# Kernel tuning notes

Hardware: AMD Instinct MI355X
Metric: run time of the kernel (lower is better)

The kernel has to match this reference:

```python
import math
import jax, jax.numpy as jnp
import numpy as np

B, S, HID = 2, 2048, 1024
H, D = 16, 64
LOG2E = 1.442695041


def setup_inputs() -> dict:
    key = jax.random.key(0)
    ks = jax.random.split(key, 10)
    init = lambda k, shape, fan_in: jax.random.uniform(k, shape, jnp.float32, -1.0, 1.0) / math.sqrt(fan_in)
    hidden_states = jax.random.normal(ks[0], (B, S, HID), jnp.float32)
    # additive causal mask [B, 1, S, S]: 0 on/below diagonal, large negative above
    neg = jnp.finfo(jnp.float32).min
    causal = jnp.where(jnp.tril(jnp.ones((S, S), bool)), 0.0, neg).astype(jnp.float32)
    attention_mask = jnp.broadcast_to(causal[None, None], (B, 1, S, S))
    return {
        "hidden_states": hidden_states,
        "attention_mask": attention_mask,
        "scaling": jax.random.normal(ks[1], (D,), jnp.float32) * 0.1,
        "q_w": init(ks[2], (H * D, HID), HID),
        "q_b": jnp.zeros((H * D,), jnp.float32),
        "k_w": init(ks[3], (H * D, HID), HID),
        "k_b": jnp.zeros((H * D,), jnp.float32),
        "v_w": init(ks[4], (H * D, HID), HID),
        "v_b": jnp.zeros((H * D,), jnp.float32),
        "o_w": init(ks[5], (HID, H * D), H * D),
        "o_b": jnp.zeros((HID,), jnp.float32),
    }


def reference(hidden_states, attention_mask, scaling, q_w, q_b, k_w, k_b, v_w, v_b, o_w, o_b):
    x = hidden_states  # [B, S, HID]
    def proj(w, b):
        y = jnp.einsum('bsh,oh->bso', x, w) + b          # [B, S, H*D]
        return y.reshape(B, S, H, D).transpose(0, 2, 1, 3)  # [B, H, S, D]
    q = proj(q_w, q_b)
    k = proj(k_w, k_b)
    v = proj(v_w, v_b)
    # learned per-head-dim softplus scale on queries
    scale = jax.nn.softplus(scaling) * (LOG2E / math.sqrt(D))  # [D]
    q = q * scale[None, None, None, :]
    attn = jnp.einsum('bhsd,bhtd->bhst', q, k)  # [B, H, S, S]
    attn = attn + attention_mask
    attn = jax.nn.softmax(attn.astype(jnp.float32), axis=-1).astype(q.dtype)
    # dropout p=0.0 / eval mode: no-op
    out = jnp.einsum('bhst,bhtd->bhsd', attn, v)           # [B, H, S, D]
    out = out.transpose(0, 2, 1, 3).reshape(B, S, H * D)   # [B, S, H*D]
    out = jnp.einsum('bsf,of->bso', out, o_w) + o_b        # [B, S, HID]
    return out, attn
```

## Files before the change

### kernel.cpp

```cpp
#include <hip/hip_runtime.h>
#include <hip/hip_bf16.h>

#define BATCH 2
#define SEQ   2048
#define HIDN  1024
#define NH    16
#define HD    64

typedef __attribute__((ext_vector_type(8))) short short8;
typedef __attribute__((ext_vector_type(4))) float floatx4;
typedef __attribute__((ext_vector_type(8))) unsigned short ushort8;

__device__ __forceinline__ unsigned short f2bf(float f) {
    union { float f; unsigned int u; } v; v.f = f;
    unsigned int u = v.u;
    u += 0x7fffu + ((u >> 16) & 1u);
    return (unsigned short)(u >> 16);
}

__device__ __forceinline__ ushort8 pack16(float4 f0, float4 f1) {
    ushort8 r;
    r[0] = f2bf(f0.x); r[1] = f2bf(f0.y); r[2] = f2bf(f0.z); r[3] = f2bf(f0.w);
    r[4] = f2bf(f1.x); r[5] = f2bf(f1.y); r[6] = f2bf(f1.z); r[7] = f2bf(f1.w);
    return r;
}

__global__ __launch_bounds__(256) void qkv_kernel(
    const float* __restrict__ x,
    const float* __restrict__ qw, const float* __restrict__ qbias,
    const float* __restrict__ kw, const float* __restrict__ kbias,
    const float* __restrict__ vw, const float* __restrict__ vbias,
    const float* __restrict__ scaling,
    unsigned short* __restrict__ qo,
    unsigned short* __restrict__ ko,
    unsigned short* __restrict__ vo)
{
    const int z = blockIdx.z;
    const float* w    = (z == 0) ? qw : (z == 1) ? kw : vw;
    const float* bias = (z == 0) ? qbias : (z == 1) ? kbias : vbias;
    unsigned short* dst = (z == 0) ? qo : (z == 1) ? ko : vo;

    const int n0 = blockIdx.x * 128;
    const int m0 = blockIdx.y * 128;
    const int tid  = threadIdx.x;
    const int lane = tid & 63;
    const int wv   = tid >> 6;
    const int nidx = lane & 15;
    const int quad = lane >> 4;

    __shared__ unsigned short As[128][40];
    __shared__ unsigned short Bs[128][40];

    floatx4 acc[2][8];
#pragma unroll
    for (int rt = 0; rt < 2; rt++)
#pragma unroll
        for (int ct = 0; ct < 8; ct++) acc[rt][ct] = (floatx4)0.0f;

    const int srow = tid >> 1;
    const int scol = (tid & 1) * 16;

    for (int k0 = 0; k0 < HIDN; k0 += 32) {
        __syncthreads();
        {
            const float4* g = (const float4*)(x + (size_t)(m0 + srow) * HIDN + k0 + scol);
            float4 f0 = g[0], f1 = g[1], f2 = g[2], f3 = g[3];
            *(ushort8*)&As[srow][scol]     = pack16(f0, f1);
            *(ushort8*)&As[srow][scol + 8] = pack16(f2, f3);
        }
        {
            const float4* g = (const float4*)(w + (size_t)(n0 + srow) * HIDN + k0 + scol);
            float4 f0 = g[0], f1 = g[1], f2 = g[2], f3 = g[3];
            *(ushort8*)&Bs[srow][scol]     = pack16(f0, f1);
            *(ushort8*)&Bs[srow][scol + 8] = pack16(f2, f3);
        }
        __syncthreads();

        short8 a[2], bb[8];
#pragma unroll
        for (int rt = 0; rt < 2; rt++)
            a[rt] = *(const short8*)&As[wv * 32 + rt * 16 + nidx][quad * 8];
#pragma unroll
        for (int ct = 0; ct < 8; ct++)
            bb[ct] = *(const short8*)&Bs[ct * 16 + nidx][quad * 8];
#pragma unroll
        for (int rt = 0; rt < 2; rt++)
#pragma unroll
            for (int ct = 0; ct < 8; ct++)
                acc[rt][ct] = __builtin_amdgcn_mfma_f32_16x16x32_bf16(a[rt], bb[ct], acc[rt][ct], 0, 0, 0);
    }

    const float sconst = 1.442695041f / 8.0f;
#pragma unroll
    for (int ct = 0; ct < 8; ct++) {
        int col = n0 + ct * 16 + nidx;
        float bcol = bias[col];
        float mult = 1.0f;
        if (z == 0) {
            float sc = scaling[col & (HD - 1)];
            mult = __logf(1.0f + __expf(sc)) * sconst;
        }
#pragma unroll
        for (int rt = 0; rt < 2; rt++) {
#pragma unroll
            for (int rg = 0; rg < 4; rg++) {
                int row = m0 + wv * 32 + rt * 16 + quad * 4 + rg;
                float val = (acc[rt][ct][rg] + bcol) * mult;
                int b_ = row >> 11, s_ = row & (SEQ - 1);
                int h_ = col >> 6,  d_ = col & (HD - 1);
                dst[((size_t)(b_ * NH + h_) * SEQ + s_) * HD + d_] = f2bf(val);
            }
        }
    }
}

__global__ __launch_bounds__(256) void attn_kernel(
    const unsigned short* __restrict__ q,
    const unsigned short* __restrict__ k,
    const unsigned short* __restrict__ v,
    float* __restrict__ attn,
    unsigned short* __restrict__ ctx)
{
    const int qt = blockIdx.x;
    const int h  = blockIdx.y;
    const int b  = blockIdx.z;
    const int tid  = threadIdx.x;
    const int lane = tid & 63;
    const int wv   = tid >> 6;
    const int nidx = lane & 15;
    const int quad = lane >> 4;

    const unsigned short* qg = q + (size_t)((b * NH + h) * SEQ) * HD;
    const unsigned short* kg = k + (size_t)((b * NH + h) * SEQ) * HD;
    const unsigned short* vg = v + (size_t)((b * NH + h) * SEQ) * HD;
    float* ag = attn + (size_t)(b * NH + h) * SEQ * SEQ;

    __shared__ unsigned short Qs[64][72];
    __shared__ unsigned short Ks[64][72];
    __shared__ unsigned short Vs[64][72];
    __shared__ unsigned short Ps[64][72];

    const int srow = tid >> 2;
    const int sseg = tid & 3;

    {
        const uint4* g = (const uint4*)(qg + (size_t)(qt * 64 + srow) * HD);
        uint4 u0 = g[sseg], u1 = g[sseg + 4];
        *(uint4*)&Qs[srow][sseg * 8]      = u0;
        *(uint4*)&Qs[srow][sseg * 8 + 32] = u1;
    }

    const int arow  = wv * 16 + nidx;
    const int crow0 = wv * 16 + quad * 4;
    const int rowg0 = qt * 64 + crow0;

    float psum[4] = {0.f, 0.f, 0.f, 0.f};
    for (int kt = 0; kt <= qt; kt++) {
        __syncthreads();
        {
            const uint4* g = (const uint4*)(kg + (size_t)(kt * 64 + srow) * HD);
            uint4 u0 = g[sseg], u1 = g[sseg + 4];
            *(uint4*)&Ks[srow][sseg * 8]      = u0;
            *(uint4*)&Ks[srow][sseg * 8 + 32] = u1;
        }
        __syncthreads();

        short8 a0 = *(const short8*)&Qs[arow][quad * 8];
        short8 a1 = *(const short8*)&Qs[arow][32 + quad * 8];
        const bool diag = (kt == qt);
#pragma unroll
        for (int ct = 0; ct < 4; ct++) {
            floatx4 sacc = (floatx4)0.0f;
            short8 b0 = *(const short8*)&Ks[ct * 16 + nidx][quad * 8];
            short8 b1 = *(const short8*)&Ks[ct * 16 + nidx][32 + quad * 8];
            sacc = __builtin_amdgcn_mfma_f32_16x16x32_bf16(a0, b0, sacc, 0, 0, 0);
            sacc = __builtin_amdgcn_mfma_f32_16x16x32_bf16(a1, b1, sacc, 0, 0, 0);
            int colg = kt * 64 + ct * 16 + nidx;
#pragma unroll
            for (int rg = 0; rg < 4; rg++) {
                float e = __expf(sacc[rg]);
                if (diag && colg > rowg0 + rg) e = 0.0f;
                psum[rg] += e;
            }
        }
    }

    float invl[4];
#pragma unroll
    for (int rg = 0; rg < 4; rg++) {
        float s = psum[rg];
        s += __shfl_xor(s, 1);
        s += __shfl_xor(s, 2);
        s += __shfl_xor(s, 4);
        s += __shfl_xor(s, 8);
        invl[rg] = 1.0f / s;
    }

    floatx4 oacc[4];
#pragma unroll
    for (int ct = 0; ct < 4; ct++) oacc[ct] = (floatx4)0.0f;

    for (int kt = 0; kt <= qt; kt++) {
        __syncthreads();
        {
            const uint4* g = (const uint4*)(kg + (size_t)(kt * 64 + srow) * HD);
            uint4 u0 = g[sseg], u1 = g[sseg + 4];
            *(uint4*)&Ks[srow][sseg * 8]      = u0;
            *(uint4*)&Ks[srow][sseg * 8 + 32] = u1;
        }
        {
            const uint4* g = (const uint4*)(vg + (size_t)(kt * 64 + srow) * HD);
            uint4 u0 = g[sseg], u1 = g[sseg + 4];
            union { uint4 u; unsigned short s[8]; } w0, w1;
            w0.u = u0; w1.u = u1;
#pragma unroll
            for (int j = 0; j < 8; j++) Vs[sseg * 8 + j][srow]      = w0.s[j];
#pragma unroll
            for (int j = 0; j < 8; j++) Vs[sseg * 8 + 32 + j][srow] = w1.s[j];
        }
        __syncthreads();

        short8 a0 = *(const short8*)&Qs[arow][quad * 8];
        short8 a1 = *(const short8*)&Qs[arow][32 + quad * 8];
        const bool diag = (kt == qt);
#pragma unroll
        for (int ct = 0; ct < 4; ct++) {
            floatx4 sacc = (floatx4)0.0f;
            short8 b0 = *(const short8*)&Ks[ct * 16 + nidx][quad * 8];
            short8 b1 = *(const short8*)&Ks[ct * 16 + nidx][32 + quad * 8];
            sacc = __builtin_amdgcn_mfma_f32_16x16x32_bf16(a0, b0, sacc, 0, 0, 0);
            sacc = __builtin_amdgcn_mfma_f32_16x16x32_bf16(a1, b1, sacc, 0, 0, 0);
            int colg = kt * 64 + ct * 16 + nidx;
#pragma unroll
            for (int rg = 0; rg < 4; rg++) {
                float e = __expf(sacc[rg]);
                if (diag && colg > rowg0 + rg) e = 0.0f;
                ag[(size_t)(rowg0 + rg) * SEQ + colg] = e * invl[rg];
                Ps[crow0 + rg][ct * 16 + nidx] = f2bf(e);
            }
        }
        __syncthreads();

#pragma unroll
        for (int ki = 0; ki < 2; ki++) {
            short8 pa = *(const short8*)&Ps[arow][ki * 32 + quad * 8];
#pragma unroll
            for (int ct = 0; ct < 4; ct++) {
                short8 vb = *(const short8*)&Vs[ct * 16 + nidx][ki * 32 + quad * 8];
                oacc[ct] = __builtin_amdgcn_mfma_f32_16x16x32_bf16(pa, vb, oacc[ct], 0, 0, 0);
            }
        }
    }

    const int zc0 = (qt + 1) * 64;
    if (zc0 < SEQ) {
        const int zw4 = (SEQ - zc0) >> 2;
        const int total = 64 * zw4;
        for (int i = tid; i < total; i += 256) {
            int r = i / zw4;
            int c = zc0 + (i - r * zw4) * 4;
            *(float4*)&ag[(size_t)(qt * 64 + r) * SEQ + c] = make_float4(0.f, 0.f, 0.f, 0.f);
        }
    }

#pragma unroll
    for (int ct = 0; ct < 4; ct++) {
#pragma unroll
        for (int rg = 0; rg < 4; rg++) {
            int rowg = rowg0 + rg;
            int d = ct * 16 + nidx;
            float val = oacc[ct][rg] * invl[rg];
            ctx[((size_t)(b * SEQ + rowg) * NH + h) * HD + d] = f2bf(val);
        }
    }
}

__global__ __launch_bounds__(256) void oproj_kernel(
    const unsigned short* __restrict__ ctx,
    const float* __restrict__ ow, const float* __restrict__ ob,
    float* __restrict__ out)
{
    const int n0 = blockIdx.x * 128;
    const int m0 = blockIdx.y * 128;
    const int tid  = threadIdx.x;
    const int lane = tid & 63;
    const int wv   = tid >> 6;
    const int nidx = lane & 15;
    const int quad = lane >> 4;

    __shared__ unsigned short As[128][40];
    __shared__ unsigned short Bs[128][40];

    floatx4 acc[2][8];
#pragma unroll
    for (int rt = 0; rt < 2; rt++)
#pragma unroll
        for (int ct = 0; ct < 8; ct++) acc[rt][ct] = (floatx4)0.0f;

    const int srow = tid >> 1;
    const int scol = (tid & 1) * 16;

    for (int k0 = 0; k0 < HIDN; k0 += 32) {
        __syncthreads();
        {
            const uint4* g = (const uint4*)(ctx + (size_t)(m0 + srow) * HIDN + k0 + scol);
            uint4 u0 = g[0], u1 = g[1];
            *(uint4*)&As[srow][scol]     = u0;
            *(uint4*)&As[srow][scol + 8] = u1;
        }
        {
            const float4* g = (const float4*)(ow + (size_t)(n0 + srow) * HIDN + k0 + scol);
            float4 f0 = g[0], f1 = g[1], f2 = g[2], f3 = g[3];
            *(ushort8*)&Bs[srow][scol]     = pack16(f0, f1);
            *(ushort8*)&Bs[srow][scol + 8] = pack16(f2, f3);
        }
        __syncthreads();

        short8 a[2], bb[8];
#pragma unroll
        for (int rt = 0; rt < 2; rt++)
            a[rt] = *(const short8*)&As[wv * 32 + rt * 16 + nidx][quad * 8];
#pragma unroll
        for (int ct = 0; ct < 8; ct++)
            bb[ct] = *(const short8*)&Bs[ct * 16 + nidx][quad * 8];
#pragma unroll
        for (int rt = 0; rt < 2; rt++)
#pragma unroll
            for (int ct = 0; ct < 8; ct++)
                acc[rt][ct] = __builtin_amdgcn_mfma_f32_16x16x32_bf16(a[rt], bb[ct], acc[rt][ct], 0, 0, 0);
    }

#pragma unroll
    for (int ct = 0; ct < 8; ct++) {
        int col = n0 + ct * 16 + nidx;
        float bcol = ob[col];
#pragma unroll
        for (int rt = 0; rt < 2; rt++) {
#pragma unroll
            for (int rg = 0; rg < 4; rg++) {
                int row = m0 + wv * 32 + rt * 16 + quad * 4 + rg;
                out[(size_t)row * HIDN + col] = acc[rt][ct][rg] + bcol;
            }
        }
    }
}

extern "C" void kernel_launch(void* const* d_in, const int* in_sizes, int n_in,
                              void* d_out, int out_size, void* d_ws, size_t ws_size,
                              hipStream_t stream) {
    const float* x       = (const float*)d_in[0];
    const float* scaling = (const float*)d_in[2];
    const float* qw = (const float*)d_in[3];
    const float* qb = (const float*)d_in[4];
    const float* kw = (const float*)d_in[5];
    const float* kb = (const float*)d_in[6];
    const float* vw = (const float*)d_in[7];
    const float* vb = (const float*)d_in[8];
    const float* ow = (const float*)d_in[9];
    const float* ob = (const float*)d_in[10];

    float* out  = (float*)d_out;
    float* attn = out + (size_t)BATCH * SEQ * HIDN;

    const size_t per = (size_t)BATCH * NH * SEQ * HD;
    unsigned short* qbuf = (unsigned short*)d_ws;
    unsigned short* kbuf = qbuf + per;
    unsigned short* vbuf = kbuf + per;
    unsigned short* ctxb = vbuf + per;

    qkv_kernel<<<dim3(8, 32, 3), 256, 0, stream>>>(
        x, qw, qb, kw, kb, vw, vb, scaling, qbuf, kbuf, vbuf);
    attn_kernel<<<dim3(32, NH, BATCH), 256, 0, stream>>>(
        qbuf, kbuf, vbuf, attn, ctxb);
    oproj_kernel<<<dim3(8, 32), 256, 0, stream>>>(
        ctxb, ow, ob, out);
}
```

Measured before the change: 799.5 us.

## Pre-convert to bf16, unify GEMMs with direct-to-LDS swizzled loads, transpose V

Adds a conversion kernel that casts the input and all weights to bf16 once. A templated GEMM replaces both projection kernels; it stages tiles with global_load_lds into an XOR-swizzled LDS layout using K-steps of 64, and writes V transposed. The attention kernel drops LDS staging of Q/K/V and reads fragments straight from global memory, replacing barriers with compiler fences, and zero-fills the masked region row-wise per wave. This aims to cut conversion work, LDS traffic and synchronisation, at the cost of an extra kernel pass and uncoalesced global fragment reads. Removing the barriers around the shared Ps buffer is safe only because each wave writes and reads its own rows.

```diff
diff --git a/kernel.cpp b/kernel.cpp
--- a/kernel.cpp
+++ b/kernel.cpp
@@ -9,7 +9,6 @@
 
 typedef __attribute__((ext_vector_type(8))) short short8;
 typedef __attribute__((ext_vector_type(4))) float floatx4;
-typedef __attribute__((ext_vector_type(8))) unsigned short ushort8;
 
 __device__ __forceinline__ unsigned short f2bf(float f) {
     union { float f; unsigned int u; } v; v.f = f;
@@ -18,97 +17,173 @@
     return (unsigned short)(u >> 16);
 }
 
-__device__ __forceinline__ ushort8 pack16(float4 f0, float4 f1) {
-    ushort8 r;
-    r[0] = f2bf(f0.x); r[1] = f2bf(f0.y); r[2] = f2bf(f0.z); r[3] = f2bf(f0.w);
-    r[4] = f2bf(f1.x); r[5] = f2bf(f1.y); r[6] = f2bf(f1.z); r[7] = f2bf(f1.w);
-    return r;
-}
-
-__global__ __launch_bounds__(256) void qkv_kernel(
-    const float* __restrict__ x,
-    const float* __restrict__ qw, const float* __restrict__ qbias,
-    const float* __restrict__ kw, const float* __restrict__ kbias,
-    const float* __restrict__ vw, const float* __restrict__ vbias,
+__device__ __forceinline__ void glds16(const unsigned short* g, unsigned short* l) {
+    typedef const unsigned int __attribute__((address_space(1)))* gp_t;
+    typedef unsigned int __attribute__((address_space(3)))* lp_t;
+    __builtin_amdgcn_global_load_lds((gp_t)(const void*)g, (lp_t)(void*)l, 16, 0, 0);
+}
+
+__global__ __launch_bounds__(256) void convert_kernel(
+    const float* __restrict__ x,  const float* __restrict__ qw,
+    const float* __restrict__ kw, const float* __restrict__ vw,
+    const float* __restrict__ ow, unsigned short* __restrict__ dst)
+{
+    size_t i = ((size_t)blockIdx.x * 256 + threadIdx.x) * 4;
+    const float* src;
+    if (i < 4194304) {
+        src = x + i;
+    } else {
+        size_t w = i - 4194304;
+        int seg = (int)(w >> 20);
+        size_t o = w & 1048575;
+        src = (seg == 0 ? qw : seg == 1 ? kw : seg == 2 ? vw : ow) + o;
+    }
+    float4 f = *(const float4*)src;
+    ushort4 u;
+    u.x = f2bf(f.x); u.y = f2bf(f.y); u.z = f2bf(f.z); u.w = f2bf(f.w);
+    *(ushort4*)(dst + i) = u;
+}
+
+template<int MT>
+__global__ __launch_bounds__(256) void gemm_kernel(
+    const unsigned short* __restrict__ A,
+    const unsigned short* __restrict__ w0, const unsigned short* __restrict__ w1,
+    const unsigned short* __restrict__ w2,
+    const float* __restrict__ bias0, const float* __restrict__ bias1,
+    const float* __restrict__ bias2,
     const float* __restrict__ scaling,
-    unsigned short* __restrict__ qo,
-    unsigned short* __restrict__ ko,
-    unsigned short* __restrict__ vo)
+    unsigned short* __restrict__ o0, unsigned short* __restrict__ o1,
+    unsigned short* __restrict__ o2,
+    float* __restrict__ ofp,
+    int modebase)
 {
-    const int z = blockIdx.z;
-    const float* w    = (z == 0) ? qw : (z == 1) ? kw : vw;
-    const float* bias = (z == 0) ? qbias : (z == 1) ? kbias : vbias;
-    unsigned short* dst = (z == 0) ? qo : (z == 1) ? ko : vo;
+    constexpr int RT = MT / 64;
+    constexpr int IA = MT / 32;
+    const int mode = modebase + blockIdx.z;
+    const unsigned short* W = (mode == 1) ? w1 : (mode == 2) ? w2 : w0;
+    const float* bias = (mode == 1) ? bias1 : (mode == 2) ? bias2 : bias0;
 
     const int n0 = blockIdx.x * 128;
-    const int m0 = blockIdx.y * 128;
-    const int tid  = threadIdx.x;
+    const int m0 = blockIdx.y * MT;
+    const int tid = threadIdx.x;
     const int lane = tid & 63;
-    const int wv   = tid >> 6;
+    const int wv = tid >> 6;
     const int nidx = lane & 15;
     const int quad = lane >> 4;
 
-    __shared__ unsigned short As[128][40];
-    __shared__ unsigned short Bs[128][40];
-
-    floatx4 acc[2][8];
-#pragma unroll
-    for (int rt = 0; rt < 2; rt++)
+    __shared__ unsigned short As[MT * 64];
+    __shared__ unsigned short Bs[128 * 64];
+
+    floatx4 acc[RT][8];
+#pragma unroll
+    for (int rt = 0; rt < RT; rt++)
 #pragma unroll
         for (int ct = 0; ct < 8; ct++) acc[rt][ct] = (floatx4)0.0f;
 
-    const int srow = tid >> 1;
-    const int scol = (tid & 1) * 16;
-
-    for (int k0 = 0; k0 < HIDN; k0 += 32) {
+    const bool vswap = (mode == 2);
+
+    for (int k0 = 0; k0 < HIDN; k0 += 64) {
         __syncthreads();
-        {
-            const float4* g = (const float4*)(x + (size_t)(m0 + srow) * HIDN + k0 + scol);
-            float4 f0 = g[0], f1 = g[1], f2 = g[2], f3 = g[3];
-            *(ushort8*)&As[srow][scol]     = pack16(f0, f1);
-            *(ushort8*)&As[srow][scol + 8] = pack16(f2, f3);
-        }
-        {
-            const float4* g = (const float4*)(w + (size_t)(n0 + srow) * HIDN + k0 + scol);
-            float4 f0 = g[0], f1 = g[1], f2 = g[2], f3 = g[3];
-            *(ushort8*)&Bs[srow][scol]     = pack16(f0, f1);
-            *(ushort8*)&Bs[srow][scol + 8] = pack16(f2, f3);
+#pragma unroll
+        for (int i = 0; i < IA; i++) {
+            int c = (wv * IA + i) * 64 + lane;
+            int r = c >> 3;
+            int qq = (c & 7) ^ (r & 7);
+            glds16(A + (size_t)(m0 + r) * HIDN + k0 + qq * 8,
+                   As + (size_t)(wv * IA + i) * 512);
+        }
+#pragma unroll
+        for (int i = 0; i < 4; i++) {
+            int c = (wv * 4 + i) * 64 + lane;
+            int r = c >> 3;
+            int qq = (c & 7) ^ (r & 7);
+            glds16(W + (size_t)(n0 + r) * HIDN + k0 + qq * 8,
+                   Bs + (size_t)(wv * 4 + i) * 512);
         }
         __syncthreads();
 
-        short8 a[2], bb[8];
-#pragma unroll
-        for (int rt = 0; rt < 2; rt++)
-            a[rt] = *(const short8*)&As[wv * 32 + rt * 16 + nidx][quad * 8];
-#pragma unroll
-        for (int ct = 0; ct < 8; ct++)
-            bb[ct] = *(const short8*)&Bs[ct * 16 + nidx][quad * 8];
-#pragma unroll
-        for (int rt = 0; rt < 2; rt++)
-#pragma unroll
-            for (int ct = 0; ct < 8; ct++)
-                acc[rt][ct] = __builtin_amdgcn_mfma_f32_16x16x32_bf16(a[rt], bb[ct], acc[rt][ct], 0, 0, 0);
+#pragma unroll
+        for (int kc = 0; kc < 2; kc++) {
+            short8 a[RT];
+#pragma unroll
+            for (int rt = 0; rt < RT; rt++) {
+                int r = wv * (MT / 4) + rt * 16 + nidx;
+                int qq = kc * 4 + quad;
+                int chunk = r * 8 + (qq ^ (r & 7));
+                a[rt] = *(const short8*)(As + chunk * 8);
+            }
+            if (vswap) {
+#pragma unroll
+                for (int ct = 0; ct < 8; ct++) {
+                    int r = ct * 16 + nidx;
+                    int qq = kc * 4 + quad;
+                    int chunk = r * 8 + (qq ^ (r & 7));
+                    short8 bf = *(const short8*)(Bs + chunk * 8);
+#pragma unroll
+                    for (int rt = 0; rt < RT; rt++)
+                        acc[rt][ct] = __builtin_amdgcn_mfma_f32_16x16x32_bf16(bf, a[rt], acc[rt][ct], 0, 0, 0);
+                }
+            } else {
+#pragma unroll
+                for (int ct = 0; ct < 8; ct++) {
+                    int r = ct * 16 + nidx;
+                    int qq = kc * 4 + quad;
+                    int chunk = r * 8 + (qq ^ (r & 7));
+                    short8 bf = *(const short8*)(Bs + chunk * 8);
+#pragma unroll
+                    for (int rt = 0; rt < RT; rt++)
+                        acc[rt][ct] = __builtin_amdgcn_mfma_f32_16x16x32_bf16(a[rt], bf, acc[rt][ct], 0, 0, 0);
+                }
+            }
+        }
     }
 
     const float sconst = 1.442695041f / 8.0f;
 #pragma unroll
     for (int ct = 0; ct < 8; ct++) {
-        int col = n0 + ct * 16 + nidx;
-        float bcol = bias[col];
-        float mult = 1.0f;
-        if (z == 0) {
-            float sc = scaling[col & (HD - 1)];
-            mult = __logf(1.0f + __expf(sc)) * sconst;
-        }
-#pragma unroll
-        for (int rt = 0; rt < 2; rt++) {
-#pragma unroll
-            for (int rg = 0; rg < 4; rg++) {
-                int row = m0 + wv * 32 + rt * 16 + quad * 4 + rg;
-                float val = (acc[rt][ct][rg] + bcol) * mult;
-                int b_ = row >> 11, s_ = row & (SEQ - 1);
-                int h_ = col >> 6,  d_ = col & (HD - 1);
-                dst[((size_t)(b_ * NH + h_) * SEQ + s_) * HD + d_] = f2bf(val);
+        if (mode == 2) {
+#pragma unroll
+            for (int rt = 0; rt < RT; rt++) {
+#pragma unroll
+                for (int rg = 0; rg < 4; rg++) {
+                    int wrow = n0 + ct * 16 + quad * 4 + rg;
+                    int xrow = m0 + wv * (MT / 4) + rt * 16 + nidx;
+                    float val = acc[rt][ct][rg] + bias[wrow];
+                    int h_ = wrow >> 6, d_ = wrow & (HD - 1);
+                    int b_ = xrow >> 11, s_ = xrow & (SEQ - 1);
+                    o2[((size_t)(b_ * NH + h_) * HD + d_) * SEQ + s_] = f2bf(val);
+                }
+            }
+        } else if (mode == 3) {
+            int col = n0 + ct * 16 + nidx;
+            float bc = bias[col];
+#pragma unroll
+            for (int rt = 0; rt < RT; rt++) {
+#pragma unroll
+                for (int rg = 0; rg < 4; rg++) {
+                    int row = m0 + wv * (MT / 4) + rt * 16 + quad * 4 + rg;
+                    ofp[(size_t)row * HIDN + col] = acc[rt][ct][rg] + bc;
+                }
+            }
+        } else {
+            int col = n0 + ct * 16 + nidx;
+            float bc = bias[col];
+            float mult = 1.0f;
+            if (mode == 0) {
+                float sc = scaling[col & (HD - 1)];
+                mult = __logf(1.0f + __expf(sc)) * sconst;
+            }
+            unsigned short* dst = (mode == 0) ? o0 : o1;
+#pragma unroll
+            for (int rt = 0; rt < RT; rt++) {
+#pragma unroll
+                for (int rg = 0; rg < 4; rg++) {
+                    int row = m0 + wv * (MT / 4) + rt * 16 + quad * 4 + rg;
+                    float val = (acc[rt][ct][rg] + bc) * mult;
+                    int b_ = row >> 11, s_ = row & (SEQ - 1);
+                    int h_ = col >> 6,  d_ = col & (HD - 1);
+                    dst[((size_t)(b_ * NH + h_) * SEQ + s_) * HD + d_] = f2bf(val);
+                }
             }
         }
     }
@@ -117,7 +192,7 @@
 __global__ __launch_bounds__(256) void attn_kernel(
     const unsigned short* __restrict__ q,
     const unsigned short* __restrict__ k,
-    const unsigned short* __restrict__ v,
+    const unsigned short* __restrict__ vT,
     float* __restrict__ attn,
     unsigned short* __restrict__ ctx)
 {
@@ -125,54 +200,35 @@
     const int h  = blockIdx.y;
     const int b  = blockIdx.z;
     const int tid  = threadIdx.x;
+    const int wv   = (tid >> 6);
     const int lane = tid & 63;
-    const int wv   = tid >> 6;
     const int nidx = lane & 15;
     const int quad = lane >> 4;
 
-    const unsigned short* qg = q + (size_t)((b * NH + h) * SEQ) * HD;
-    const unsigned short* kg = k + (size_t)((b * NH + h) * SEQ) * HD;
-    const unsigned short* vg = v + (size_t)((b * NH + h) * SEQ) * HD;
+    const unsigned short* qg = q  + (size_t)((b * NH + h) * SEQ) * HD;
+    const unsigned short* kg = k  + (size_t)((b * NH + h) * SEQ) * HD;
+    const unsigned short* vg = vT + (size_t)((b * NH + h) * HD) * SEQ;
     float* ag = attn + (size_t)(b * NH + h) * SEQ * SEQ;
 
-    __shared__ unsigned short Qs[64][72];
-    __shared__ unsigned short Ks[64][72];
-    __shared__ unsigned short Vs[64][72];
     __shared__ unsigned short Ps[64][72];
-
-    const int srow = tid >> 2;
-    const int sseg = tid & 3;
-
-    {
-        const uint4* g = (const uint4*)(qg + (size_t)(qt * 64 + srow) * HD);
-        uint4 u0 = g[sseg], u1 = g[sseg + 4];
-        *(uint4*)&Qs[srow][sseg * 8]      = u0;
-        *(uint4*)&Qs[srow][sseg * 8 + 32] = u1;
-    }
 
     const int arow  = wv * 16 + nidx;
     const int crow0 = wv * 16 + quad * 4;
     const int rowg0 = qt * 64 + crow0;
 
+    const unsigned short* qrow = qg + (size_t)(qt * 64 + arow) * HD + quad * 8;
+    short8 a0 = *(const short8*)qrow;
+    short8 a1 = *(const short8*)(qrow + 32);
+
     float psum[4] = {0.f, 0.f, 0.f, 0.f};
     for (int kt = 0; kt <= qt; kt++) {
-        __syncthreads();
-        {
-            const uint4* g = (const uint4*)(kg + (size_t)(kt * 64 + srow) * HD);
-            uint4 u0 = g[sseg], u1 = g[sseg + 4];
-            *(uint4*)&Ks[srow][sseg * 8]      = u0;
-            *(uint4*)&Ks[srow][sseg * 8 + 32] = u1;
-        }
-        __syncthreads();
-
-        short8 a0 = *(const short8*)&Qs[arow][quad * 8];
-        short8 a1 = *(const short8*)&Qs[arow][32 + quad * 8];
         const bool diag = (kt == qt);
 #pragma unroll
         for (int ct = 0; ct < 4; ct++) {
+            const unsigned short* kr = kg + (size_t)(kt * 64 + ct * 16 + nidx) * HD + quad * 8;
+            short8 b0 = *(const short8*)kr;
+            short8 b1 = *(const short8*)(kr + 32);
             floatx4 sacc = (floatx4)0.0f;
-            short8 b0 = *(const short8*)&Ks[ct * 16 + nidx][quad * 8];
-            short8 b1 = *(const short8*)&Ks[ct * 16 + nidx][32 + quad * 8];
             sacc = __builtin_amdgcn_mfma_f32_16x16x32_bf16(a0, b0, sacc, 0, 0, 0);
             sacc = __builtin_amdgcn_mfma_f32_16x16x32_bf16(a1, b1, sacc, 0, 0, 0);
             int colg = kt * 64 + ct * 16 + nidx;
@@ -201,33 +257,13 @@
     for (int ct = 0; ct < 4; ct++) oacc[ct] = (floatx4)0.0f;
 
     for (int kt = 0; kt <= qt; kt++) {
-        __syncthreads();
-        {
-            const uint4* g = (const uint4*)(kg + (size_t)(kt * 64 + srow) * HD);
-            uint4 u0 = g[sseg], u1 = g[sseg + 4];
-            *(uint4*)&Ks[srow][sseg * 8]      = u0;
-            *(uint4*)&Ks[srow][sseg * 8 + 32] = u1;
-        }
-        {
-            const uint4* g = (const uint4*)(vg + (size_t)(kt * 64 + srow) * HD);
-            uint4 u0 = g[sseg], u1 = g[sseg + 4];
-            union { uint4 u; unsigned short s[8]; } w0, w1;
-            w0.u = u0; w1.u = u1;
-#pragma unroll
-            for (int j = 0; j < 8; j++) Vs[sseg * 8 + j][srow]      = w0.s[j];
-#pragma unroll
-            for (int j = 0; j < 8; j++) Vs[sseg * 8 + 32 + j][srow] = w1.s[j];
-        }
-        __syncthreads();
-
-        short8 a0 = *(const short8*)&Qs[arow][quad * 8];
-        short8 a1 = *(const short8*)&Qs[arow][32 + quad * 8];
         const bool diag = (kt == qt);
 #pragma unroll
         for (int ct = 0; ct < 4; ct++) {
+            const unsigned short* kr = kg + (size_t)(kt * 64 + ct * 16 + nidx) * HD + quad * 8;
+            short8 b0 = *(const short8*)kr;
+            short8 b1 = *(const short8*)(kr + 32);
             floatx4 sacc = (floatx4)0.0f;
-            short8 b0 = *(const short8*)&Ks[ct * 16 + nidx][quad * 8];
-            short8 b1 = *(const short8*)&Ks[ct * 16 + nidx][32 + quad * 8];
             sacc = __builtin_amdgcn_mfma_f32_16x16x32_bf16(a0, b0, sacc, 0, 0, 0);
             sacc = __builtin_amdgcn_mfma_f32_16x16x32_bf16(a1, b1, sacc, 0, 0, 0);
             int colg = kt * 64 + ct * 16 + nidx;
@@ -239,27 +275,28 @@
                 Ps[crow0 + rg][ct * 16 + nidx] = f2bf(e);
             }
         }
-        __syncthreads();
+        asm volatile("" ::: "memory");
 
 #pragma unroll
         for (int ki = 0; ki < 2; ki++) {
             short8 pa = *(const short8*)&Ps[arow][ki * 32 + quad * 8];
 #pragma unroll
             for (int ct = 0; ct < 4; ct++) {
-                short8 vb = *(const short8*)&Vs[ct * 16 + nidx][ki * 32 + quad * 8];
+                const unsigned short* vr = vg + (size_t)(ct * 16 + nidx) * SEQ + kt * 64 + ki * 32 + quad * 8;
+                short8 vb = *(const short8*)vr;
                 oacc[ct] = __builtin_amdgcn_mfma_f32_16x16x32_bf16(pa, vb, oacc[ct], 0, 0, 0);
             }
         }
-    }
-
-    const int zc0 = (qt + 1) * 64;
-    if (zc0 < SEQ) {
-        const int zw4 = (SEQ - zc0) >> 2;
-        const int total = 64 * zw4;
-        for (int i = tid; i < total; i += 256) {
-            int r = i / zw4;
-            int c = zc0 + (i - r * zw4) * 4;
-            *(float4*)&ag[(size_t)(qt * 64 + r) * SEQ + c] = make_float4(0.f, 0.f, 0.f, 0.f);
+        asm volatile("" ::: "memory");
+    }
+
+    {
+        const int c4start = (qt + 1) * 16;
+        const float4 z4 = make_float4(0.f, 0.f, 0.f, 0.f);
+        for (int r = wv; r < 64; r += 4) {
+            float4* rowp = (float4*)(ag + (size_t)(qt * 64 + r) * SEQ);
+            for (int c4 = c4start + lane; c4 < 512; c4 += 64)
+                rowp[c4] = z4;
         }
     }
 
@@ -271,76 +308,6 @@
             int d = ct * 16 + nidx;
             float val = oacc[ct][rg] * invl[rg];
             ctx[((size_t)(b * SEQ + rowg) * NH + h) * HD + d] = f2bf(val);
-        }
-    }
-}
-
-__global__ __launch_bounds__(256) void oproj_kernel(
-    const unsigned short* __restrict__ ctx,
-    const float* __restrict__ ow, const float* __restrict__ ob,
-    float* __restrict__ out)
-{
-    const int n0 = blockIdx.x * 128;
-    const int m0 = blockIdx.y * 128;
-    const int tid  = threadIdx.x;
-    const int lane = tid & 63;
-    const int wv   = tid >> 6;
-    const int nidx = lane & 15;
-    const int quad = lane >> 4;
-
-    __shared__ unsigned short As[128][40];
-    __shared__ unsigned short Bs[128][40];
-
-    floatx4 acc[2][8];
-#pragma unroll
-    for (int rt = 0; rt < 2; rt++)
-#pragma unroll
-        for (int ct = 0; ct < 8; ct++) acc[rt][ct] = (floatx4)0.0f;
-
-    const int srow = tid >> 1;
-    const int scol = (tid & 1) * 16;
-
-    for (int k0 = 0; k0 < HIDN; k0 += 32) {
-        __syncthreads();
-        {
-            const uint4* g = (const uint4*)(ctx + (size_t)(m0 + srow) * HIDN + k0 + scol);
-            uint4 u0 = g[0], u1 = g[1];
-            *(uint4*)&As[srow][scol]     = u0;
-            *(uint4*)&As[srow][scol + 8] = u1;
-        }
-        {
-            const float4* g = (const float4*)(ow + (size_t)(n0 + srow) * HIDN + k0 + scol);
-            float4 f0 = g[0], f1 = g[1], f2 = g[2], f3 = g[3];
-            *(ushort8*)&Bs[srow][scol]     = pack16(f0, f1);
-            *(ushort8*)&Bs[srow][scol + 8] = pack16(f2, f3);
-        }
-        __syncthreads();
-
-        short8 a[2], bb[8];
-#pragma unroll
-        for (int rt = 0; rt < 2; rt++)
-            a[rt] = *(const short8*)&As[wv * 32 + rt * 16 + nidx][quad * 8];
-#pragma unroll
-        for (int ct = 0; ct < 8; ct++)
-            bb[ct] = *(const short8*)&Bs[ct * 16 + nidx][quad * 8];
-#pragma unroll
-        for (int rt = 0; rt < 2; rt++)
-#pragma unroll
-            for (int ct = 0; ct < 8; ct++)
-                acc[rt][ct] = __builtin_amdgcn_mfma_f32_16x16x32_bf16(a[rt], bb[ct], acc[rt][ct], 0, 0, 0);
-    }
-
-#pragma unroll
-    for (int ct = 0; ct < 8; ct++) {
-        int col = n0 + ct * 16 + nidx;
-        float bcol = ob[col];
-#pragma unroll
-        for (int rt = 0; rt < 2; rt++) {
-#pragma unroll
-            for (int rg = 0; rg < 4; rg++) {
-                int row = m0 + wv * 32 + rt * 16 + quad * 4 + rg;
-                out[(size_t)row * HIDN + col] = acc[rt][ct][rg] + bcol;
-            }
         }
     }
 }
@@ -362,16 +329,26 @@
     float* out  = (float*)d_out;
     float* attn = out + (size_t)BATCH * SEQ * HIDN;
 
-    const size_t per = (size_t)BATCH * NH * SEQ * HD;
-    unsigned short* qbuf = (unsigned short*)d_ws;
-    unsigned short* kbuf = qbuf + per;
-    unsigned short* vbuf = kbuf + per;
-    unsigned short* ctxb = vbuf + per;
-
-    qkv_kernel<<<dim3(8, 32, 3), 256, 0, stream>>>(
-        x, qw, qb, kw, kb, vw, vb, scaling, qbuf, kbuf, vbuf);
+    unsigned short* xbf  = (unsigned short*)d_ws;
+    unsigned short* qwb  = xbf + 4194304;
+    unsigned short* kwb  = qwb + 1048576;
+    unsigned short* vwb  = kwb + 1048576;
+    unsigned short* owb  = vwb + 1048576;
+    unsigned short* qbuf = owb + 1048576;
+    unsigned short* kbuf = qbuf + 4194304;
+    unsigned short* vTb  = kbuf + 4194304;
+    unsigned short* ctxb = vTb + 4194304;
+
+    convert_kernel<<<8192, 256, 0, stream>>>(x, qw, kw, vw, ow, xbf);
+
+    gemm_kernel<128><<<dim3(8, 32, 3), 256, 0, stream>>>(
+        xbf, qwb, kwb, vwb, qb, kb, vb, scaling,
+        qbuf, kbuf, vTb, nullptr, 0);
+
     attn_kernel<<<dim3(32, NH, BATCH), 256, 0, stream>>>(
-        qbuf, kbuf, vbuf, attn, ctxb);
-    oproj_kernel<<<dim3(8, 32), 256, 0, stream>>>(
-        ctxb, ow, ob, out);
-}
+        qbuf, kbuf, vTb, attn, ctxb);
+
+    gemm_kernel<64><<<dim3(8, 64, 1), 256, 0, stream>>>(
+        ctxb, owb, owb, owb, ob, ob, ob, scaling,
+        nullptr, nullptr, nullptr, out, 3);
+}
```

After: 947.9 us. +18.6%, slower.
